# Performance work log

Measured on AMD Instinct MI355X. Metric: run time of the kernel, lower is better.

Reference implementation:

```python
import jax, jax.numpy as jnp
import numpy as np

N = 16384      # nodes
E = 262144     # edges (avg degree 16)
R = 9          # relation types
D_IN = 384     # embed_size
D_H = 768      # hidden_size
N_CLASSES = 5


def setup_inputs() -> dict:
    key = jax.random.key(0)
    ks = jax.random.split(key, 11)
    s = 0.02
    return {
        "x": jax.random.normal(ks[0], (N, D_IN), jnp.float32),
        "edge_index": jax.random.randint(ks[1], (2, E), 0, N, dtype=jnp.int64)
        if jax.config.jax_enable_x64 else jax.random.randint(ks[1], (2, E), 0, N).astype(jnp.int32),
        "edge_type": jax.random.randint(ks[2], (E,), 0, R).astype(jnp.int32),
        "rel_W": jax.random.normal(ks[3], (R, D_H, D_IN), jnp.float32) * s,
        "rel_b": jax.random.normal(ks[4], (R, D_H), jnp.float32) * s,
        "norm_constants": jnp.ones((R,), jnp.float32),
        "mp_lin_W": jax.random.normal(ks[5], (D_H, D_H), jnp.float32) * s,
        "mp_lin_b": jax.random.normal(ks[6], (D_H,), jnp.float32) * s,
        "mp_self_W": jax.random.normal(ks[7], (D_H, D_H), jnp.float32) * s,
        "mp_self_b": jax.random.normal(ks[8], (D_H,), jnp.float32) * s,
        "out_W": jax.random.normal(ks[9], (N_CLASSES, D_H), jnp.float32) * s,
        "out_b": jax.random.normal(ks[10], (N_CLASSES,), jnp.float32) * s,
    }


def reference(x, edge_index, edge_type, rel_W, rel_b, norm_constants,
              mp_lin_W, mp_lin_b, mp_self_W, mp_self_b, out_W, out_b):
    n = x.shape[0]
    src = edge_index[0]  # j : message source (x_j)
    dst = edge_index[1]  # i : aggregation target

    # --- RelationAwareMP ---
    # edge_weights[i, j] from x @ x.T, computed per edge (identical math)
    ew = jnp.einsum('ed,ed->e', x[dst], x[src])                  # [E]
    norm = ew / norm_constants[edge_type]                        # [E]
    # per-relation linear applied to all nodes, then gathered per edge
    h = jnp.einsum('nd,rhd->rnh', x, rel_W) + rel_b[:, None, :]  # [R,N,H]
    msg = h[edge_type, src]                                      # [E,H]
    aggr = jax.ops.segment_sum(norm[:, None] * msg, dst, num_segments=n)
    x1 = jax.nn.relu(aggr)                                       # [N,H]

    # --- MP (add aggregation + self transform) ---
    self_x = x1 @ mp_self_W.T + mp_self_b
    hm = x1 @ mp_lin_W.T + mp_lin_b
    aggr2 = jax.ops.segment_sum(hm[src], dst, num_segments=n)
    x2 = jax.nn.relu(aggr2 + self_x)                             # [N,H]

    # --- readout ---
    pooled = x2.mean(axis=0)                                     # [H]
    return pooled @ out_W.T + out_b                              # [N_CLASSES]
```

## Files before the change

kernel.cpp:

```cpp
#include <hip/hip_runtime.h>

typedef unsigned char  u8;
typedef unsigned short u16;
typedef unsigned int   u32;

#define NN   16384
#define EE   262144
#define RR   9
#define DIN  384
#define DH   768
#define KSU  3456
#define KS   3488
#define NPB  4
#define PCOP 16

typedef float  f32x4 __attribute__((ext_vector_type(4)));
typedef float  f32x2 __attribute__((ext_vector_type(2)));
typedef u32    u32x2 __attribute__((ext_vector_type(2)));
typedef __bf16 b16x8 __attribute__((ext_vector_type(8)));

__device__ __forceinline__ u16 f2bf(float f){
  u32 u = __builtin_bit_cast(u32, f);
  u += 0x7fffu + ((u >> 16) & 1u);
  return (u16)(u >> 16);
}
__device__ __forceinline__ float bf2f(u16 h){
  u32 u = ((u32)h) << 16;
  return __builtin_bit_cast(float, u);
}
__device__ __forceinline__ u32 pkbf(float a, float b){
  return (u32)f2bf(a) | ((u32)f2bf(b) << 16);
}
__device__ __forceinline__ void gll16(const void* g, void* l){
  __builtin_amdgcn_global_load_lds((const __attribute__((address_space(1))) void*)g,
                                   (__attribute__((address_space(3))) void*)l, 16, 0, 0);
}
template<int N> __device__ __forceinline__ float dppror(float v){
  return __builtin_bit_cast(float,
    __builtin_amdgcn_update_dpp(0, __builtin_bit_cast(int, v), 0x120+N, 0xF, 0xF, true));
}
__device__ __forceinline__ float swz16(float v){
  return __builtin_bit_cast(float,
    __builtin_amdgcn_ds_swizzle(__builtin_bit_cast(int, v), 0x401F));
}

__global__ void k_count(const int* __restrict__ dst, int* __restrict__ counts){
  const int e = blockIdx.x*256 + threadIdx.x;
  if (e < EE) atomicAdd(&counts[dst[e]], 1);
}

__global__ __launch_bounds__(1024) void k_scan(const int* __restrict__ counts,
                                               int* __restrict__ starts,
                                               int* __restrict__ cursor){
  __shared__ int tot[1024];
  const int t = threadIdx.x;
  int loc[16]; int s = 0;
  #pragma unroll
  for (int j=0;j<16;j++){ loc[j] = counts[t*16+j]; s += loc[j]; }
  tot[t] = s;
  __syncthreads();
  for (int o=1;o<1024;o<<=1){
    int v = (t>=o) ? tot[t-o] : 0;
    __syncthreads();
    tot[t] += v;
    __syncthreads();
  }
  int run = tot[t] - s;
  #pragma unroll
  for (int j=0;j<16;j++){ starts[t*16+j] = run; cursor[t*16+j] = run; run += loc[j]; }
  if (t == 1023) starts[NN] = run;
}

__global__ void k_place(const int* __restrict__ src, const int* __restrict__ dst,
                        const int* __restrict__ et, int* __restrict__ cursor,
                        int* __restrict__ sp){
  const int e = blockIdx.x*256 + threadIdx.x;
  if (e < EE){
    const int p = atomicAdd(&cursor[dst[e]], 1);
    sp[p] = (int)(((u32)et[e] << 28) | (u32)src[e]);
  }
}

__global__ void k_convW1(const float* __restrict__ rW, const float* __restrict__ rb,
                         u16* __restrict__ Wst){
  const int hh = blockIdx.y;
  const int k  = blockIdx.x*256 + threadIdx.x;
  if (k >= KS) return;
  float v;
  if (k < KSU){ const int r = k / DIN; const int d = k - r*DIN;
                v = rW[((long)r*DH + hh)*DIN + d]; }
  else if (k < KSU + RR){ const int r = k - KSU; v = rb[(long)r*DH + hh]; }
  else v = 0.f;
  Wst[(long)hh*KS + k] = f2bf(v);
}

__global__ void k_convW2(const float* __restrict__ lW, const float* __restrict__ sW,
                         u16* __restrict__ WB){
  const int idx = blockIdx.x*256 + threadIdx.x;
  const float v = (idx < DH*DH) ? lW[idx] : sW[idx - DH*DH];
  WB[idx] = f2bf(v);
}

__global__ __launch_bounds__(256, 3) void k_phase1f(const float* __restrict__ x,
                                                    const int* __restrict__ sp,
                                                    const float* __restrict__ nc,
                                                    const int* __restrict__ starts,
                                                    u16* __restrict__ s){
  const int wv = threadIdx.x >> 6;
  const int l  = threadIdx.x & 63;
  const int i  = blockIdx.x*4 + wv;
  const float* xdp = x + (long)i*DIN;
  const f32x4 xq = *(const f32x4*)(xdp + 4*l);
  const f32x2 xr = *(const f32x2*)(xdp + 256 + 2*l);
  float acc[RR][6];
  float cacc[RR];
  #pragma unroll
  for (int r=0;r<RR;r++){
    cacc[r] = 0.f;
    #pragma unroll
    for (int j=0;j<6;j++) acc[r][j] = 0.f;
  }
  const int e0 = starts[i], e1 = starts[i+1];
  f32x4 Aq={0,0,0,0}, Bq={0,0,0,0}, Cq={0,0,0,0}, Dq={0,0,0,0};
  f32x2 Ar={0,0}, Br={0,0}, Cr={0,0}, Dr={0,0};
  u32 qA=0,qB=0,qC=0,qD=0;
  #define LDE(S, QQ, IDX) { const int pe_=(IDX); if (pe_ < e1){ QQ = (u32)sp[pe_]; \
      const float* xs_ = x + (long)(QQ & 0x3FFFu)*DIN; \
      S##q = *(const f32x4*)(xs_ + 4*l); \
      S##r = *(const f32x2*)(xs_ + 256 + 2*l); } }
  LDE(A,qA,e0) LDE(B,qB,e0+1) LDE(C,qC,e0+2) LDE(D,qD,e0+3)
  #define DOT(uq,ur) (xq.x*uq.x + xq.y*uq.y + xq.z*uq.z + xq.w*uq.w \
                    + xr.x*ur.x + xr.y*ur.y)
  #define UPD(R,P,cq,cr) { cacc[R] += P; \
      acc[R][0] += P*cq.x; acc[R][1] += P*cq.y; acc[R][2] += P*cq.z; \
      acc[R][3] += P*cq.w; acc[R][4] += P*cr.x; acc[R][5] += P*cr.y; }
  #define SW(RQ,P,cq,cr) switch (RQ){ \
      case 0: UPD(0,P,cq,cr); break; case 1: UPD(1,P,cq,cr); break; \
      case 2: UPD(2,P,cq,cr); break; case 3: UPD(3,P,cq,cr); break; \
      case 4: UPD(4,P,cq,cr); break; case 5: UPD(5,P,cq,cr); break; \
      case 6: UPD(6,P,cq,cr); break; case 7: UPD(7,P,cq,cr); break; \
      default: UPD(8,P,cq,cr); break; }
  for (int p=e0; p<e1; p+=4){
    const f32x4 aq=Aq, bq=Bq, cq=Cq, dq=Dq;
    const f32x2 ar=Ar, br=Br, cr=Cr, dr=Dr;
    const u32 qa=qA, qb=qB, qc=qC, qd=qD;
    const bool h1 = p+1<e1, h2 = p+2<e1, h3 = p+3<e1;
    LDE(A,qA,p+4) LDE(B,qB,p+5) LDE(C,qC,p+6) LDE(D,qD,p+7)
    float pa = DOT(aq,ar), pb = DOT(bq,br);
    float pc = DOT(cq,cr), pd = DOT(dq,dr);
    pa += dppror<1>(pa); pb += dppror<1>(pb); pc += dppror<1>(pc); pd += dppror<1>(pd);
    pa += dppror<2>(pa); pb += dppror<2>(pb); pc += dppror<2>(pc); pd += dppror<2>(pd);
    pa += dppror<4>(pa); pb += dppror<4>(pb); pc += dppror<4>(pc); pd += dppror<4>(pd);
    pa += dppror<8>(pa); pb += dppror<8>(pb); pc += dppror<8>(pc); pd += dppror<8>(pd);
    pa += swz16(pa); pb += swz16(pb); pc += swz16(pc); pd += swz16(pd);
    pa += __shfl_xor(pa,32); pb += __shfl_xor(pb,32);
    pc += __shfl_xor(pc,32); pd += __shfl_xor(pd,32);
    SW(qa>>28, pa, aq,ar);
    if (h1){ SW(qb>>28, pb, bq,br); }
    if (h2){ SW(qc>>28, pc, cq,cr); }
    if (h3){ SW(qd>>28, pd, dq,dr); }
  }
  #undef LDE
  #undef DOT
  #undef UPD
  #undef SW
  u16* srow = s + (long)i*KS;
  #pragma unroll
  for (int r=0;r<RR;r++){
    const float inv = 1.0f / nc[r];
    const u32 pk0 = pkbf(acc[r][0]*inv, acc[r][1]*inv);
    const u32 pk1 = pkbf(acc[r][2]*inv, acc[r][3]*inv);
    const u32 pk2 = pkbf(acc[r][4]*inv, acc[r][5]*inv);
    *(u32x2*)(srow + r*DIN + 4*l) = (u32x2){pk0, pk1};
    ((u32*)(srow + r*DIN + 256))[l] = pk2;
  }
  float cv = 0.f;
  #pragma unroll
  for (int r=0;r<RR;r++) cv = (l == r) ? cacc[r] : cv;
  if (l < 32){
    const float invl = (l < RR) ? 1.0f/nc[l] : 0.f;
    srow[KSU + l] = f2bf(l < RR ? cv*invl : 0.f);
  }
}

template<int MODE, int NT>
__global__ __launch_bounds__(512, 2)
void k_gemm256(const u16* __restrict__ A, const u16* __restrict__ B, int K,
               u16* __restrict__ O0, u16* __restrict__ O1,
               const float* __restrict__ b0, const float* __restrict__ b1)
{
  __shared__ __align__(16) u16 lds[4][2][256*32];
  const int cpx = gridDim.x >> 3;
  const int bid = blockIdx.x;
  const int lg  = (bid & 7)*cpx + (bid >> 3);
  const int mt  = lg / NT;
  const long m0 = (long)mt * 256;
  const long n0 = (long)(lg - mt*NT) * 256;
  const int t   = threadIdx.x;
  const int wv  = t >> 6;
  const int ln  = t & 63;
  const int wm  = wv >> 2;
  const int wn  = wv & 3;
  const int fr  = ln & 15, fq = ln >> 4;

  const int lrow  = t >> 2;
  const int gslot = (t & 3) ^ ((lrow >> 1) & 3);

  f32x4 acc[8][4];
  #pragma unroll
  for (int i=0;i<8;i++)
    #pragma unroll
    for (int j=0;j<4;j++) acc[i][j] = {0.f,0.f,0.f,0.f};

  const int nk = K >> 5;

  #define STAGE(TT) { const int tt_ = (TT); const long k0_ = (long)tt_*32;          \
    u16* sa_ = &lds[tt_ & 3][0][0]; u16* sb_ = &lds[tt_ & 3][1][0];                 \
    gll16(A + (m0 +       lrow)*(long)K + k0_ + gslot*8, sa_ + wv*512);             \
    gll16(A + (m0 + 128 + lrow)*(long)K + k0_ + gslot*8, sa_ + 4096 + wv*512);      \
    gll16(B + (n0 +       lrow)*(long)K + k0_ + gslot*8, sb_ + wv*512);             \
    gll16(B + (n0 + 128 + lrow)*(long)K + k0_ + gslot*8, sb_ + 4096 + wv*512); }

  STAGE(0) STAGE(1) STAGE(2)
  asm volatile("s_waitcnt vmcnt(8)" ::: "memory");
  __builtin_amdgcn_s_barrier();

  for (int tt = 0; tt < nk; ++tt){
    if (tt + 3 < nk) STAGE(tt + 3)
    const u16* sa = &lds[tt & 3][0][0];
    const u16* sb = &lds[tt & 3][1][0];
    b16x8 av[8], bv[4];
    #pragma unroll
    for (int i=0;i<8;i++){
      const int row = wm*128 + i*16 + fr;
      av[i] = *(const b16x8*)((const u8*)sa + row*64 + ((fq ^ ((row>>1)&3)) << 4));
    }
    #pragma unroll
    for (int j=0;j<4;j++){
      const int row = wn*64 + j*16 + fr;
      bv[j] = *(const b16x8*)((const u8*)sb + row*64 + ((fq ^ ((row>>1)&3)) << 4));
    }
    __builtin_amdgcn_s_setprio(1);
    #pragma unroll
    for (int i=0;i<8;i++)
      #pragma unroll
      for (int j=0;j<4;j++)
        acc[i][j] = __builtin_amdgcn_mfma_f32_16x16x32_bf16(av[i], bv[j], acc[i][j], 0, 0, 0);
    __builtin_amdgcn_s_setprio(0);
    if (tt + 3 < nk)      asm volatile("s_waitcnt vmcnt(8)" ::: "memory");
    else if (tt + 2 < nk) asm volatile("s_waitcnt vmcnt(4)" ::: "memory");
    else if (tt + 1 < nk) asm volatile("s_waitcnt vmcnt(0)" ::: "memory");
    __builtin_amdgcn_s_barrier();
  }
  #undef STAGE

  #pragma unroll
  for (int i=0;i<8;i++){
    #pragma unroll
    for (int j=0;j<4;j++){
      #pragma unroll
      for (int r=0;r<4;r++){
        const long m = m0 + wm*128 + i*16 + fq*4 + r;
        const long n = n0 + wn*64  + j*16 + fr;
        float v = acc[i][j][r];
        if (MODE == 0){
          v = v > 0.f ? v : 0.f;
          O0[m*DH + n] = f2bf(v);
        } else {
          if (n < DH) O0[m*DH + n]      = f2bf(v + b0[n]);
          else        O1[m*DH + (n-DH)] = f2bf(v + b1[n-DH]);
        }
      }
    }
  }
}

__global__ __launch_bounds__(128) void k_phase2(const u16* __restrict__ hm,
                                                const u16* __restrict__ sfx,
                                                const int* __restrict__ sp,
                                                const int* __restrict__ starts,
                                                float* __restrict__ pooledP){
  const int t  = threadIdx.x;
  const int i0 = blockIdx.x * NPB;
  const int p0 = starts[i0];
  const int pend = starts[i0 + NPB];
  u32 sf00,sf01,sf02, sf10,sf11,sf12, sf20,sf21,sf22, sf30,sf31,sf32;
  { const u32* sr = (const u32*)(sfx + (long)(i0+0)*DH); sf00=sr[t]; sf01=sr[t+128]; sf02=sr[t+256]; }
  { const u32* sr = (const u32*)(sfx + (long)(i0+1)*DH); sf10=sr[t]; sf11=sr[t+128]; sf12=sr[t+256]; }
  { const u32* sr = (const u32*)(sfx + (long)(i0+2)*DH); sf20=sr[t]; sf21=sr[t+128]; sf22=sr[t+256]; }
  { const u32* sr = (const u32*)(sfx + (long)(i0+3)*DH); sf30=sr[t]; sf31=sr[t+128]; sf32=sr[t+256]; }
  u32 A0=0,A1=0,A2=0,B0=0,B1=0,B2=0,C0=0,C1=0,C2=0,D0=0,D1=0,D2=0;
  u32 E0=0,E1=0,E2=0,F0=0,F1=0,F2=0,G0=0,G1=0,G2=0,H0=0,H1=0,H2=0;
  #define PLD(S, IDX) { const int nf_=(IDX); if (nf_ < pend){ \
      const u32* hr_ = (const u32*)(hm + (long)(((u32)sp[nf_]) & 0x3FFFu)*DH); \
      S##0=hr_[t]; S##1=hr_[t+128]; S##2=hr_[t+256]; } }
  PLD(A,p0)   PLD(B,p0+1) PLD(C,p0+2) PLD(D,p0+3)
  PLD(E,p0+4) PLD(F,p0+5) PLD(G,p0+6) PLD(H,p0+7)
  float a0=0.f,a1=0.f,a2=0.f,a3=0.f,a4=0.f,a5=0.f;
  float q0=0.f,q1=0.f,q2=0.f,q3=0.f,q4=0.f,q5=0.f;
  int i = i0;
  int e1 = starts[i0+1];
  #define FLUSH(K) { float v_; \
    v_=a0+bf2f((u16)sf##K##0);        q0+=fmaxf(v_,0.f); \
    v_=a1+bf2f((u16)(sf##K##0>>16));  q1+=fmaxf(v_,0.f); \
    v_=a2+bf2f((u16)sf##K##1);        q2+=fmaxf(v_,0.f); \
    v_=a3+bf2f((u16)(sf##K##1>>16));  q3+=fmaxf(v_,0.f); \
    v_=a4+bf2f((u16)sf##K##2);        q4+=fmaxf(v_,0.f); \
    v_=a5+bf2f((u16)(sf##K##2>>16));  q5+=fmaxf(v_,0.f); \
    a0=a1=a2=a3=a4=a5=0.f; }
  #define FLUSHI { switch (i - i0){ case 0: FLUSH(0); break; case 1: FLUSH(1); break; \
                   case 2: FLUSH(2); break; default: FLUSH(3); break; } }
  while (i < i0+NPB && e1 == p0){ FLUSHI; ++i; e1 = (i < i0+NPB) ? starts[i+1] : 0x7fffffff; }
  #define STEP(S, K) { const int pe_ = base + K; if (pe_ < pend){ \
      const u32 d0_=S##0, d1_=S##1, d2_=S##2; \
      PLD(S, pe_ + 8); \
      a0+=bf2f((u16)d0_); a1+=bf2f((u16)(d0_>>16)); \
      a2+=bf2f((u16)d1_); a3+=bf2f((u16)(d1_>>16)); \
      a4+=bf2f((u16)d2_); a5+=bf2f((u16)(d2_>>16)); \
      while (i < i0+NPB && pe_+1 == e1){ FLUSHI; ++i; \
        e1 = (i < i0+NPB) ? starts[i+1] : 0x7fffffff; } } }
  for (int base = p0; base < pend; base += 8){
    STEP(A,0) STEP(B,1) STEP(C,2) STEP(D,3)
    STEP(E,4) STEP(F,5) STEP(G,6) STEP(H,7)
  }
  while (i < i0+NPB){ FLUSHI; ++i; }
  #undef PLD
  #undef FLUSH
  #undef FLUSHI
  #undef STEP
  float* pd = pooledP + (blockIdx.x & (PCOP-1)) * DH;
  atomicAdd(&pd[2*t],       q0);
  atomicAdd(&pd[2*t+1],     q1);
  atomicAdd(&pd[256+2*t],   q2);
  atomicAdd(&pd[256+2*t+1], q3);
  atomicAdd(&pd[512+2*t],   q4);
  atomicAdd(&pd[512+2*t+1], q5);
}

__global__ __launch_bounds__(256) void k_final(const float* __restrict__ pooledP,
                                               const float* __restrict__ oW,
                                               const float* __restrict__ ob,
                                               float* __restrict__ out){
  __shared__ float ps[DH];
  __shared__ float red[256];
  const int t = threadIdx.x;
  for (int h=t; h<DH; h+=256){
    float s = 0.f;
    #pragma unroll
    for (int c=0;c<PCOP;c++) s += pooledP[c*DH + h];
    ps[h] = s;
  }
  __syncthreads();
  for (int c=0;c<5;c++){
    float p = 0.f;
    for (int h=t; h<DH; h+=256) p += ps[h]*oW[c*DH + h];
    red[t] = p; __syncthreads();
    for (int o=128;o;o>>=1){ if (t<o) red[t]+=red[t+o]; __syncthreads(); }
    if (t == 0) out[c] = red[0]*(1.f/(float)NN) + ob[c];
    __syncthreads();
  }
}

extern "C" void kernel_launch(void* const* d_in, const int* in_sizes, int n_in,
                              void* d_out, int out_size, void* d_ws, size_t ws_size,
                              hipStream_t stream)
{
  (void)in_sizes; (void)n_in; (void)out_size; (void)ws_size;
  const float* x     = (const float*)d_in[0];
  const int*   ei    = (const int*)  d_in[1];
  const int*   et    = (const int*)  d_in[2];
  const float* relW  = (const float*)d_in[3];
  const float* relb  = (const float*)d_in[4];
  const float* nc    = (const float*)d_in[5];
  const float* linW  = (const float*)d_in[6];
  const float* linb  = (const float*)d_in[7];
  const float* selfW = (const float*)d_in[8];
  const float* selfb = (const float*)d_in[9];
  const float* outW  = (const float*)d_in[10];
  const float* outb  = (const float*)d_in[11];
  float* out = (float*)d_out;

  u8* w = (u8*)d_ws;
  int*   counts = (int*)(w + 0);
  int*   starts = (int*)(w + 65536);
  int*   cursor = (int*)(w + 131328);
  int*   srcp   = (int*)(w + 196864);
  u16*   Wst    = (u16*)(w + 4391168);
  u16*   WB     = (u16*)(w + 9748736);
  u16*   x1     = (u16*)(w + 12108032);
  u16*   S      = (u16*)(w + 37276928);
  u16*   hm     = S;
  u16*   sfx    = (u16*)(w + 37276928 + 25165824);
  float* pooledP = (float*)(w + 37276928 + 50331648);

  const int* esrc = ei;
  const int* edst = ei + EE;

  hipMemsetAsync(counts, 0, NN*sizeof(int), stream);

  k_count <<<EE/256, 256, 0, stream>>>(edst, counts);
  k_scan  <<<1, 1024, 0, stream>>>(counts, starts, cursor);
  k_place <<<EE/256, 256, 0, stream>>>(esrc, edst, et, cursor, srcp);
  k_convW1<<<dim3(14, DH), 256, 0, stream>>>(relW, relb, Wst);
  k_convW2<<<(2*DH*DH)/256, 256, 0, stream>>>(linW, selfW, WB);
  k_phase1f<<<NN/4, 256, 0, stream>>>(x, srcp, nc, starts, S);
  k_gemm256<0,3><<<(NN/256)*(DH/256), 512, 0, stream>>>(
      S, Wst, KS, x1, (u16*)nullptr, (const float*)nullptr, (const float*)nullptr);
  hipMemsetAsync(pooledP, 0, PCOP*DH*sizeof(float), stream);
  k_gemm256<1,6><<<(NN/256)*(2*DH/256), 512, 0, stream>>>(
      x1, WB, DH, hm, sfx, linb, selfb);
  k_phase2<<<NN/NPB, 128, 0, stream>>>(hm, sfx, srcp, starts, pooledP);
  k_final <<<1, 256, 0, stream>>>(pooledP, outW, outb, out);
}
```

Measured before the change: 448.5 us.

## Use 256x192 GEMM tiles with 5-stage pipeline and split A/B loader waves

```diff
diff --git a/kernel.cpp b/kernel.cpp
--- a/kernel.cpp
+++ b/kernel.cpp
@@ -185,17 +185,17 @@
 
 template<int MODE, int NT>
 __global__ __launch_bounds__(512, 2)
-void k_gemm256(const u16* __restrict__ A, const u16* __restrict__ B, int K,
-               u16* __restrict__ O0, u16* __restrict__ O1,
-               const float* __restrict__ b0, const float* __restrict__ b1)
+void k_gemmw(const u16* __restrict__ A, const u16* __restrict__ B, int K,
+             u16* __restrict__ O0, u16* __restrict__ O1,
+             const float* __restrict__ b0, const float* __restrict__ b1)
 {
-  __shared__ __align__(16) u16 lds[4][2][256*32];
+  __shared__ __align__(16) u16 lds[5][14336];
   const int cpx = gridDim.x >> 3;
   const int bid = blockIdx.x;
   const int lg  = (bid & 7)*cpx + (bid >> 3);
   const int mt  = lg / NT;
   const long m0 = (long)mt * 256;
-  const long n0 = (long)(lg - mt*NT) * 256;
+  const long n0 = (long)(lg - mt*NT) * 192;
   const int t   = threadIdx.x;
   const int wv  = t >> 6;
   const int ln  = t & 63;
@@ -203,65 +203,77 @@
   const int wn  = wv & 3;
   const int fr  = ln & 15, fq = ln >> 4;
 
-  const int lrow  = t >> 2;
-  const int gslot = (t & 3) ^ ((lrow >> 1) & 3);
-
-  f32x4 acc[8][4];
+  const int u_  = t & 255;
+  const int gsl = (u_ & 3) ^ ((u_ >> 3) & 3);
+  const int sr0 = u_ >> 2;
+
+  const int su  = fq ^ ((fr >> 1) & 3);
+  const int dsA = (wm*128 + fr)*64 + (su << 4);
+  const int dsB = 16384 + (wn*48 + fr)*64 + (su << 4);
+
+  f32x4 acc[8][3];
   #pragma unroll
   for (int i=0;i<8;i++)
     #pragma unroll
-    for (int j=0;j<4;j++) acc[i][j] = {0.f,0.f,0.f,0.f};
+    for (int j=0;j<3;j++) acc[i][j] = {0.f,0.f,0.f,0.f};
 
   const int nk = K >> 5;
 
-  #define STAGE(TT) { const int tt_ = (TT); const long k0_ = (long)tt_*32;          \
-    u16* sa_ = &lds[tt_ & 3][0][0]; u16* sb_ = &lds[tt_ & 3][1][0];                 \
-    gll16(A + (m0 +       lrow)*(long)K + k0_ + gslot*8, sa_ + wv*512);             \
-    gll16(A + (m0 + 128 + lrow)*(long)K + k0_ + gslot*8, sa_ + 4096 + wv*512);      \
-    gll16(B + (n0 +       lrow)*(long)K + k0_ + gslot*8, sb_ + wv*512);             \
-    gll16(B + (n0 + 128 + lrow)*(long)K + k0_ + gslot*8, sb_ + 4096 + wv*512); }
-
-  STAGE(0) STAGE(1) STAGE(2)
-  asm volatile("s_waitcnt vmcnt(8)" ::: "memory");
+  #define STAGE(SL, TT) { const long k0_ = (long)(TT)*32;                           \
+    u16* s_ = &lds[SL][0];                                                          \
+    if (t < 256){                                                                   \
+      gll16(A + (m0 + sr0      )*(long)K + k0_ + gsl*8, s_ + (wv*64      )*8);      \
+      gll16(A + (m0 + sr0 +  64)*(long)K + k0_ + gsl*8, s_ + (wv*64 + 256)*8);      \
+      gll16(A + (m0 + sr0 + 128)*(long)K + k0_ + gsl*8, s_ + (wv*64 + 512)*8);      \
+      gll16(A + (m0 + sr0 + 192)*(long)K + k0_ + gsl*8, s_ + (wv*64 + 768)*8);      \
+    } else {                                                                        \
+      gll16(B + (n0 + sr0      )*(long)K + k0_ + gsl*8, s_ + 8192 + ((wv-4)*64      )*8); \
+      gll16(B + (n0 + sr0 +  64)*(long)K + k0_ + gsl*8, s_ + 8192 + ((wv-4)*64 + 256)*8); \
+      gll16(B + (n0 + sr0 + 128)*(long)K + k0_ + gsl*8, s_ + 8192 + ((wv-4)*64 + 512)*8); \
+    } }
+
+  #define WAITN(N4, N3) { if (wv < 4) asm volatile("s_waitcnt vmcnt(" #N4 ")" ::: "memory"); \
+                          else        asm volatile("s_waitcnt vmcnt(" #N3 ")" ::: "memory"); }
+
+  STAGE(0, 0) STAGE(1, 1) STAGE(2, 2) STAGE(3, 3)
+  WAITN(12, 9)
   __builtin_amdgcn_s_barrier();
 
+  int cs = 0, ps = 4;
   for (int tt = 0; tt < nk; ++tt){
-    if (tt + 3 < nk) STAGE(tt + 3)
-    const u16* sa = &lds[tt & 3][0][0];
-    const u16* sb = &lds[tt & 3][1][0];
-    b16x8 av[8], bv[4];
-    #pragma unroll
-    for (int i=0;i<8;i++){
-      const int row = wm*128 + i*16 + fr;
-      av[i] = *(const b16x8*)((const u8*)sa + row*64 + ((fq ^ ((row>>1)&3)) << 4));
-    }
-    #pragma unroll
-    for (int j=0;j<4;j++){
-      const int row = wn*64 + j*16 + fr;
-      bv[j] = *(const b16x8*)((const u8*)sb + row*64 + ((fq ^ ((row>>1)&3)) << 4));
-    }
+    if (tt + 4 < nk) STAGE(ps, tt + 4)
+    const u8* sl = (const u8*)&lds[cs][0];
+    b16x8 av[8], bv[3];
+    #pragma unroll
+    for (int i=0;i<8;i++) av[i] = *(const b16x8*)(sl + dsA + i*1024);
+    #pragma unroll
+    for (int j=0;j<3;j++) bv[j] = *(const b16x8*)(sl + dsB + j*1024);
     __builtin_amdgcn_s_setprio(1);
     #pragma unroll
     for (int i=0;i<8;i++)
       #pragma unroll
-      for (int j=0;j<4;j++)
+      for (int j=0;j<3;j++)
         acc[i][j] = __builtin_amdgcn_mfma_f32_16x16x32_bf16(av[i], bv[j], acc[i][j], 0, 0, 0);
     __builtin_amdgcn_s_setprio(0);
-    if (tt + 3 < nk)      asm volatile("s_waitcnt vmcnt(8)" ::: "memory");
-    else if (tt + 2 < nk) asm volatile("s_waitcnt vmcnt(4)" ::: "memory");
-    else if (tt + 1 < nk) asm volatile("s_waitcnt vmcnt(0)" ::: "memory");
+    if (tt + 4 < nk)      WAITN(12, 9)
+    else if (tt + 3 < nk) WAITN(8, 6)
+    else if (tt + 2 < nk) WAITN(4, 3)
+    else if (tt + 1 < nk) WAITN(0, 0)
     __builtin_amdgcn_s_barrier();
+    cs = (cs == 4) ? 0 : cs + 1;
+    ps = (ps == 4) ? 0 : ps + 1;
   }
   #undef STAGE
+  #undef WAITN
 
   #pragma unroll
   for (int i=0;i<8;i++){
     #pragma unroll
-    for (int j=0;j<4;j++){
+    for (int j=0;j<3;j++){
       #pragma unroll
       for (int r=0;r<4;r++){
         const long m = m0 + wm*128 + i*16 + fq*4 + r;
-        const long n = n0 + wn*64  + j*16 + fr;
+        const long n = n0 + wn*48  + j*16 + fr;
         float v = acc[i][j][r];
         if (MODE == 0){
           v = v > 0.f ? v : 0.f;
@@ -404,10 +416,10 @@
   k_convW1<<<dim3(14, DH), 256, 0, stream>>>(relW, relb, Wst);
   k_convW2<<<(2*DH*DH)/256, 256, 0, stream>>>(linW, selfW, WB);
   k_phase1f<<<NN/4, 256, 0, stream>>>(x, srcp, nc, starts, S);
-  k_gemm256<0,3><<<(NN/256)*(DH/256), 512, 0, stream>>>(
+  k_gemmw<0,4><<<(NN/256)*(DH/192), 512, 0, stream>>>(
       S, Wst, KS, x1, (u16*)nullptr, (const float*)nullptr, (const float*)nullptr);
   hipMemsetAsync(pooledP, 0, PCOP*DH*sizeof(float), stream);
-  k_gemm256<1,6><<<(NN/256)*(2*DH/256), 512, 0, stream>>>(
+  k_gemmw<1,8><<<(NN/256)*(2*DH/192), 512, 0, stream>>>(
       x1, WB, DH, hm, sfx, linb, selfb);
   k_phase2<<<NN/NPB, 128, 0, stream>>>(hm, sfx, srcp, starts, pooledP);
   k_final <<<1, 256, 0, stream>>>(pooledP, outW, outb, out);
```

After: 442.0 us. About the same (-1.5%).
